# Kernel tuning notes

Hardware: AMD Instinct MI355X
Metric: run time of the kernel (lower is better)

Reference implementation:

```python
import jax, jax.numpy as jnp
import numpy as np

# ---- static config (mirrors init_kwargs) ----
B, T, H, W = 1, 3, 64, 64
NHEADS, CH = 4, 64
DIM = NHEADS * CH            # 256 = embed_dim*nheads*dim_mult
PS, WS = 7, 9                # patch size, search window
WSH = WS // 2
K_S, K_A = 16, 8             # search top-k, aggregation top-k
S0 = 2                       # stride0: query grid stride
SCALE = CH ** -0.5
NH, NW = (H - 1) // S0 + 1, (W - 1) // S0 + 1
Q = T * NH * NW              # ntotal queries


def reflect_idx(i, n):
    # dnls reflect_bounds: i<0 -> -i, i>=n -> 2(n-1)-i
    i = jnp.where(i < 0, -i, i)
    return jnp.where(i >= n, 2 * (n - 1) - i, i)


def sepconv(x, dw, pw, b):
    # ConvQKV branch: depthwise 3x3 + pointwise 1x1 (+bias). x: [N,C,H,W]
    y = jax.lax.conv_general_dilated(x, dw, (1, 1), 'SAME',
            dimension_numbers=('NCHW', 'OIHW', 'NCHW'),
            feature_group_count=x.shape[1])
    y = jax.lax.conv_general_dilated(y, pw, (1, 1), 'SAME',
            dimension_numbers=('NCHW', 'OIHW', 'NCHW'))
    return y + b[None, :, None, None]


def setup_inputs() -> dict:
    key = jax.random.key(0)
    ks = jax.random.split(key, 12)
    p = lambda k, s, sc=0.02: jax.random.normal(k, s, jnp.float32) * sc
    z = lambda s: jnp.zeros(s, jnp.float32)
    return {
        'vid':  jax.random.normal(ks[0], (B, T, DIM, H, W), jnp.float32),
        'q_dw': p(ks[1], (DIM, 1, 3, 3), 0.1), 'q_pw': p(ks[2], (DIM, DIM, 1, 1)), 'q_b': z((DIM,)),
        'k_dw': p(ks[3], (DIM, 1, 3, 3), 0.1), 'k_pw': p(ks[4], (DIM, DIM, 1, 1)), 'k_b': z((DIM,)),
        'v_dw': p(ks[5], (DIM, 1, 3, 3), 0.1), 'v_pw': p(ks[6], (DIM, DIM, 1, 1)), 'v_b': z((DIM,)),
        'proj_w': p(ks[7], (DIM, DIM)), 'proj_b': z((DIM,)),
    }


def reference(vid, q_dw, q_pw, q_b, k_dw, k_pw, k_b, v_dw, v_pw, v_b, proj_w, proj_b):
    x = vid.reshape(B * T, DIM, H, W)
    q = (sepconv(x, q_dw, q_pw, q_b) * SCALE).reshape(B, T, NHEADS, CH, H, W)
    k = sepconv(x, k_dw, k_pw, k_b).reshape(B, T, NHEADS, CH, H, W)
    v = sepconv(x, v_dw, v_pw, v_b).reshape(B, T, NHEADS, CH, H, W)

    # ---- non-local patch search (prod_with_heads), spatial window ws x ws, wt=0 ----
    yi, xi = jnp.arange(H), jnp.arange(W)
    ye = reflect_idx(jnp.arange(H + PS - 1), H)   # reflect-extended patch footprint
    xe = reflect_idx(jnp.arange(W + PS - 1), W)

    def offset_dists(dyo, dxo):
        # pixelwise q.k for k shifted by (dyo,dxo) with reflect bounds
        ks_ = k[..., reflect_idx(yi + dyo, H), :][..., reflect_idx(xi + dxo, W)]
        d = jnp.sum(q * ks_, axis=3)              # [B,T,HD,H,W]
        # separable ps x ps patch box-sum (patch anchored top-left)
        de = d[..., ye, :][..., xe]               # [B,T,HD,H+PS-1,W+PS-1]
        dsy = sum(de[..., p:p + H, :] for p in range(PS))
        return sum(dsy[..., p:p + W] for p in range(PS))   # [B,T,HD,H,W]

    offs = jnp.arange(WS) - WSH
    dyg, dxg = jnp.meshgrid(offs, offs, indexing='ij')
    dists_all = jax.vmap(offset_dists)(dyg.ravel(), dxg.ravel())  # [L,B,T,HD,H,W]

    gy, gx = jnp.arange(0, H, S0), jnp.arange(0, W, S0)
    dg = dists_all[..., gy, :][..., gx]           # [L,B,T,HD,NH,NW]
    dists = dg.transpose(1, 3, 2, 4, 5, 0).reshape(B, NHEADS, Q, WS * WS)
    vals, inds = jax.lax.top_k(dists, K_S)        # descending
    attn = jax.nn.softmax(vals, axis=-1)[..., :K_A]  # softmax over k_s, keep top k_a
    inds = inds[..., :K_A]

    # ---- weighted patch sum (wpsum) ----
    tq = jnp.repeat(jnp.arange(T), NH * NW)       # query coords [Q]
    yq = jnp.tile(jnp.repeat(gy, NW), T)
    xq = jnp.tile(jnp.tile(gx, NH), T)
    py = jnp.arange(PS)

    vflat = v.transpose(0, 2, 3, 1, 4, 5).reshape(B, NHEADS, CH, T * H * W)
    dy_k = inds // WS - WSH
    dx_k = inds % WS - WSH

    def gather_bh(vf, li):
        # vf: [CH, T*H*W], li: [Q,PS,PS] -> [CH,Q,PS,PS]
        return vf[:, li]

    acc = jnp.zeros((B, NHEADS, CH, Q, PS, PS), vid.dtype)
    for n in range(K_A):  # small fixed loop over neighbors
        yy = reflect_idx((yq[None, None, :] + dy_k[..., n])[..., None] + py, H)  # [B,HD,Q,PS]
        xx = reflect_idx((xq[None, None, :] + dx_k[..., n])[..., None] + py, W)
        lin = tq[None, None, :, None, None] * (H * W) + yy[..., :, None] * W + xx[..., None, :]
        vp = jax.vmap(jax.vmap(gather_bh))(vflat, lin)        # [B,HD,CH,Q,PS,PS]
        acc = acc + attn[..., n][:, :, None, :, None, None] * vp

    # ---- proj over concatenated heads per (query, patch pixel) ----
    pf = acc.transpose(0, 3, 4, 5, 1, 2).reshape(-1, DIM)     # [(B Q PS PS), DIM]
    pf = pf @ proj_w.T + proj_b

    # ---- iFoldz: overlap-add + per-pixel normalization ----
    patches = pf.reshape(B, Q, PS, PS, DIM).transpose(0, 4, 1, 2, 3)  # [B,DIM,Q,PS,PS]
    yyf = reflect_idx(yq[:, None] + py, H)
    xxf = reflect_idx(xq[:, None] + py, W)
    linf = (tq[:, None, None] * (H * W) + yyf[:, :, None] * W + xxf[:, None, :]).ravel()
    vacc = jnp.zeros((B, DIM, T * H * W), vid.dtype).at[:, :, linf].add(patches.reshape(B, DIM, -1))
    zv = jnp.zeros((T * H * W,), vid.dtype).at[linf].add(1.0)
    out = (vacc / zv).reshape(B, DIM, T, H, W).transpose(0, 2, 1, 3, 4)  # [B,T,DIM,H,W]
    return out
```

## Files before the change

kernel.cpp:

```cpp
#include <hip/hip_runtime.h>
#include <hip/hip_bf16.h>
#include <cmath>

#define TT 3
#define HH 64
#define WW 64
#define NPIX 4096
#define NHEADS 4
#define CHD 64
#define DIMD 256
#define PS 7
#define WS 9
#define WSH 4
#define KS 16
#define KA 8
#define NG 32
#define QTOT 3072
#define NOFF 81
#define SCALE 0.125f

#define OFF_DW   ((size_t)0)
#define OFF_Q    ((size_t)9437184)
#define OFF_K    ((size_t)12582912)
#define OFF_V    ((size_t)15728640)
#define OFF_D    ((size_t)18874368)
#define OFF_DG   ((size_t)22855680)
#define OFF_ATTN ((size_t)23851008)
#define OFF_INDS ((size_t)23949312)
#define OFF_VACC ((size_t)24047616)

__device__ __forceinline__ int reflect_i(int i, int n) {
  i = i < 0 ? -i : i;
  return i >= n ? 2 * (n - 1) - i : i;
}

__global__ void k_dw(const float* __restrict__ vid,
                     const float* __restrict__ qdw, const float* __restrict__ kdw,
                     const float* __restrict__ vdw, float* __restrict__ dw) {
  int plane = blockIdx.x;
  int ch = plane & 255;
  const float* src = vid + (size_t)plane * NPIX;
  float wq[9], wk[9], wv[9];
#pragma unroll
  for (int i = 0; i < 9; i++) { wq[i] = qdw[ch*9+i]; wk[i] = kdw[ch*9+i]; wv[i] = vdw[ch*9+i]; }
  int x = threadIdx.x, ty = threadIdx.y;
  for (int yb = 0; yb < 16; ++yb) {
    int y = yb * 4 + ty;
    float aq = 0, ak = 0, av = 0;
#pragma unroll
    for (int a = 0; a < 3; a++) {
      int yy = y + a - 1;
      if (yy < 0 || yy >= HH) continue;
#pragma unroll
      for (int b = 0; b < 3; b++) {
        int xx = x + b - 1;
        if (xx < 0 || xx >= WW) continue;
        float xv = src[yy * WW + xx];
        aq += xv * wq[a*3+b]; ak += xv * wk[a*3+b]; av += xv * wv[a*3+b];
      }
    }
    size_t o = (size_t)plane * NPIX + y * WW + x;
    dw[o] = aq;
    dw[(size_t)3145728 + o] = ak;
    dw[(size_t)6291456 + o] = av;
  }
}

__global__ void k_pw(const float* __restrict__ dw,
                     const float* __restrict__ qpw, const float* __restrict__ qb,
                     const float* __restrict__ kpw, const float* __restrict__ kb,
                     const float* __restrict__ vpw, const float* __restrict__ vb,
                     float* __restrict__ qo, float* __restrict__ ko, float* __restrict__ vo) {
  int type = blockIdx.z / 3, t = blockIdx.z % 3;
  const float* W   = type == 0 ? qpw : (type == 1 ? kpw : vpw);
  const float* bia = type == 0 ? qb  : (type == 1 ? kb  : vb);
  const float* A = dw + (size_t)type * 3145728 + (size_t)t * 1048576;
  int p0 = blockIdx.x * 64, o0 = blockIdx.y * 64;

  __shared__ float sW[16][68];
  __shared__ float sA[16][68];

  int tid = threadIdx.x;
  int ty = tid >> 4, tx = tid & 15;
  int wrow = tid >> 2, wcol = tid & 3;
  int arow = tid >> 4, acol = tid & 15;

  float acc[4][4] = {};

  for (int k0 = 0; k0 < 256; k0 += 16) {
    float4 w4 = *(const float4*)&W[(size_t)(o0 + wrow) * 256 + k0 + wcol * 4];
    float4 a4 = *(const float4*)&A[(size_t)(k0 + arow) * NPIX + p0 + acol * 4];
    __syncthreads();
    sW[wcol * 4 + 0][wrow] = w4.x;
    sW[wcol * 4 + 1][wrow] = w4.y;
    sW[wcol * 4 + 2][wrow] = w4.z;
    sW[wcol * 4 + 3][wrow] = w4.w;
    *(float4*)&sA[arow][acol * 4] = a4;
    __syncthreads();
#pragma unroll
    for (int kk = 0; kk < 16; kk++) {
      float4 av = *(const float4*)&sW[kk][ty * 4];
      float4 bv = *(const float4*)&sA[kk][tx * 4];
      acc[0][0] += av.x * bv.x; acc[0][1] += av.x * bv.y; acc[0][2] += av.x * bv.z; acc[0][3] += av.x * bv.w;
      acc[1][0] += av.y * bv.x; acc[1][1] += av.y * bv.y; acc[1][2] += av.y * bv.z; acc[1][3] += av.y * bv.w;
      acc[2][0] += av.z * bv.x; acc[2][1] += av.z * bv.y; acc[2][2] += av.z * bv.z; acc[2][3] += av.z * bv.w;
      acc[3][0] += av.w * bv.x; acc[3][1] += av.w * bv.y; acc[3][2] += av.w * bv.z; acc[3][3] += av.w * bv.w;
    }
  }

  int obase = o0 + ty * 4, pbase = p0 + tx * 4;
  if (type == 2) {
#pragma unroll
    for (int j = 0; j < 4; j++) {
      float4 ov = make_float4(acc[0][j] + bia[obase + 0],
                              acc[1][j] + bia[obase + 1],
                              acc[2][j] + bia[obase + 2],
                              acc[3][j] + bia[obase + 3]);
      *(float4*)&vo[((size_t)t * NPIX + pbase + j) * 256 + obase] = ov;
    }
  } else {
    float* dst = (type == 0) ? qo : ko;
    float sc = (type == 0) ? SCALE : 1.0f;
#pragma unroll
    for (int i = 0; i < 4; i++) {
      float bb = bia[obase + i];
      float4 ov = make_float4((acc[i][0] + bb) * sc, (acc[i][1] + bb) * sc,
                              (acc[i][2] + bb) * sc, (acc[i][3] + bb) * sc);
      *(float4*)&dst[((size_t)t * 256 + obase + i) * NPIX + pbase] = ov;
    }
  }
}

__global__ void k_dist(const float* __restrict__ q, const float* __restrict__ k,
                       float* __restrict__ D) {
  int b = blockIdx.x;
  int y = b & 63, th = b >> 6;
  int t = th >> 2, h = th & 3;
  __shared__ float sQ[64][64];
  __shared__ float sK[64][64];
  int tid = threadIdx.x;
  int x = tid & 63, w = tid >> 6;
  const float* qp = q + ((size_t)t * 256 + h * 64) * NPIX;
  const float* kp = k + ((size_t)t * 256 + h * 64) * NPIX;
  for (int i = tid; i < 4096; i += 256)
    sQ[i >> 6][i & 63] = qp[(size_t)(i >> 6) * NPIX + y * WW + (i & 63)];
  for (int dyi = 0; dyi < 9; ++dyi) {
    int yk = reflect_i(y + dyi - 4, HH);
    __syncthreads();
    for (int i = tid; i < 4096; i += 256)
      sK[i >> 6][i & 63] = kp[(size_t)(i >> 6) * NPIX + yk * WW + (i & 63)];
    __syncthreads();
    for (int dxi = w; dxi < 9; dxi += 4) {
      int xk = reflect_i(x + dxi - 4, WW);
      float s = 0.f;
#pragma unroll 16
      for (int c = 0; c < 64; c++) s += sQ[c][x] * sK[c][xk];
      D[((size_t)(dyi * 9 + dxi) * 12 + th) * NPIX + y * WW + x] = s;
    }
  }
}

__global__ void k_box(const float* __restrict__ D, float* __restrict__ DG) {
  int th = blockIdx.x, n = blockIdx.y;
  int t = th >> 2, h = th & 3;
  __shared__ float sD[4096];
  int tid = threadIdx.x;
  const float* Dp = D + ((size_t)n * 12 + th) * NPIX;
  for (int i = tid; i < 4096; i += 256) sD[i] = Dp[i];
  __syncthreads();
  for (int qi = tid; qi < 1024; qi += 256) {
    int gy = qi >> 5, gx = qi & 31;
    int yq = gy * 2, xq = gx * 2;
    float s = 0.f;
#pragma unroll
    for (int py = 0; py < 7; py++) {
      int ry = yq + py; ry = ry >= HH ? 126 - ry : ry;
      const float* row = sD + ry * WW;
#pragma unroll
      for (int px = 0; px < 7; px++) {
        int rx = xq + px; rx = rx >= WW ? 126 - rx : rx;
        s += row[rx];
      }
    }
    DG[((size_t)h * QTOT + t * 1024 + qi) * NOFF + n] = s;
  }
}

__global__ void k_topk(const float* __restrict__ DG, float* __restrict__ attn,
                       int* __restrict__ inds) {
  int r = blockIdx.x * 256 + threadIdx.x;
  if (r >= NHEADS * QTOT) return;
  const float* row = DG + (size_t)r * NOFF;
  float dv[NOFF];
#pragma unroll
  for (int i = 0; i < NOFF; i++) dv[i] = row[i];
  float vals[KS]; int idx[KS];
#pragma unroll
  for (int s = 0; s < KS; s++) {
    float best = -1e30f; int bi = 0;
#pragma unroll
    for (int i = 0; i < NOFF; i++) {
      if (dv[i] > best) { best = dv[i]; bi = i; }
    }
    vals[s] = best; idx[s] = bi;
#pragma unroll
    for (int i = 0; i < NOFF; i++) dv[i] = (i == bi) ? -1e30f : dv[i];
  }
  float m = vals[0], den = 0.f, e[KS];
#pragma unroll
  for (int s = 0; s < KS; s++) { e[s] = expf(vals[s] - m); den += e[s]; }
  float inv = 1.f / den;
#pragma unroll
  for (int s = 0; s < KA; s++) {
    attn[(size_t)r * KA + s] = e[s] * inv;
    inds[(size_t)r * KA + s] = idx[s];
  }
}

#define NW 7
__global__ void k_agg(const float* __restrict__ v, const float* __restrict__ attn,
                      const int* __restrict__ inds, float* __restrict__ vacc) {
  int xg = blockIdx.x, y = blockIdx.y, t = blockIdx.z;
  int x0 = xg * 4;

  int g0 = max(0, (y - 5) >> 1), g1 = y >> 1;
  int ndir = g1 - g0 + 1;
  int yr = 126 - y;
  int r0 = (yr - 5) >> 1;
  int ny = ndir + (y >= 58 ? (min(31, yr >> 1) - r0 + 1) : 0);

  int gxw0 = max(0, (x0 - 5) >> 1);
  int gxw1 = (x0 + 3) >= 58 ? 31 : ((x0 + 3) >> 1);
  int nw = gxw1 - gxw0 + 1;

  __shared__ float wt[7][NW][4][8];
  __shared__ int2  rc[7][NW][4][8];

  int tid = threadIdx.x;
  {
    int iy = tid / (NW * 4);
    int rem = tid - iy * (NW * 4);
    int gxi = rem >> 2, h = rem & 3;
    if (iy < ny && gxi < nw) {
      int gy, py;
      if (iy < ndir) { gy = g0 + iy; py = y - 2 * gy; }
      else           { gy = r0 + (iy - ndir); py = yr - 2 * gy; }
      int gx = gxw0 + gxi;
      size_t r = (size_t)(h * QTOT + t * 1024 + gy * 32 + gx);
      float4 w0 = *(const float4*)(attn + r * KA);
      float4 w1 = *(const float4*)(attn + r * KA + 4);
      int4 i0 = *(const int4*)(inds + r * KA);
      int4 i1 = *(const int4*)(inds + r * KA + 4);
      int ids[8] = {i0.x, i0.y, i0.z, i0.w, i1.x, i1.y, i1.z, i1.w};
      float ww[8] = {w0.x, w0.y, w0.z, w0.w, w1.x, w1.y, w1.z, w1.w};
#pragma unroll
      for (int n = 0; n < 8; n++) {
        int dy = ids[n] / 9 - 4, dx = ids[n] % 9 - 4;
        int row = 2 * gy + dy + py;
        row = row < 0 ? -row : row;
        row = min(row, 126 - row);
        wt[iy][gxi][h][n] = ww[n];
        rc[iy][gxi][h][n] = make_int2(row << 16, 2 * gx + dx);
      }
    }
  }
  __syncthreads();

  int wv = tid >> 6, lane = tid & 63;
  int x = x0 + wv;
  int h = lane >> 4;
  const char* vB = (const char*)v + (size_t)t * ((size_t)NPIX * DIMD * 4)
                   + (unsigned)(lane * 16);

  int a0 = max(0, (x - 5) >> 1), a1 = x >> 1;
  int xr = 126 - x;
  int b0 = (xr - 5) >> 1, b1 = min(31, xr >> 1);
  bool has_refl = (x >= 58);

  float4 acc = make_float4(0.f, 0.f, 0.f, 0.f);
  for (int iy = 0; iy < ny; ++iy) {
    for (int g = a0; g <= a1; ++g) {
      int gxi = g - gxw0, px = x - 2 * g;
      const float* w8 = wt[iy][gxi][h];
      const int2* r8 = rc[iy][gxi][h];
#pragma unroll
      for (int n = 0; n < 8; n++) {
        float w = w8[n]; int2 e = r8[n];
        int col = e.y + px;
        col = col < 0 ? -col : col;
        col = min(col, 126 - col);
        float4 vv = *(const float4*)(vB + (unsigned)(e.x + (col << 10)));
        acc.x += w * vv.x; acc.y += w * vv.y; acc.z += w * vv.z; acc.w += w * vv.w;
      }
    }
    if (has_refl) {
      for (int g = b0; g <= b1; ++g) {
        int gxi = g - gxw0, px = xr - 2 * g;
        const float* w8 = wt[iy][gxi][h];
        const int2* r8 = rc[iy][gxi][h];
#pragma unroll
        for (int n = 0; n < 8; n++) {
          float w = w8[n]; int2 e = r8[n];
          int col = e.y + px;
          col = col < 0 ? -col : col;
          col = min(col, 126 - col);
          float4 vv = *(const float4*)(vB + (unsigned)(e.x + (col << 10)));
          acc.x += w * vv.x; acc.y += w * vv.y; acc.z += w * vv.z; acc.w += w * vv.w;
        }
      }
    }
  }
  float* oP = vacc + ((size_t)t * NPIX + (size_t)y * WW + x) * DIMD + lane * 4;
  *(float4*)oP = acc;
}

__device__ __forceinline__ int cov_count(int i) {
  int d = (i >> 1) - max(0, (i - 5) >> 1) + 1;
  if (i >= 58) { int r = 126 - i; d += min(31, r >> 1) - ((r - 5) >> 1) + 1; }
  return d;
}

__global__ void k_proj(const float* __restrict__ vacc,
                       const float* __restrict__ pw, const float* __restrict__ pb,
                       float* __restrict__ out) {
  int p0 = blockIdx.x * 64;
  int d0 = blockIdx.y * 64;

  __shared__ float sW[16][68];
  __shared__ float sV[16][68];

  int tid = threadIdx.x;
  int ty = tid >> 4, tx = tid & 15;
  int row = tid >> 2, col = tid & 3;

  float acc[4][4] = {};

  for (int k0 = 0; k0 < 256; k0 += 16) {
    float4 w4 = *(const float4*)&pw[(size_t)(d0 + row) * 256 + k0 + col * 4];
    float4 v4 = *(const float4*)&vacc[(size_t)(p0 + row) * 256 + k0 + col * 4];
    __syncthreads();
    sW[col * 4 + 0][row] = w4.x;
    sW[col * 4 + 1][row] = w4.y;
    sW[col * 4 + 2][row] = w4.z;
    sW[col * 4 + 3][row] = w4.w;
    sV[col * 4 + 0][row] = v4.x;
    sV[col * 4 + 1][row] = v4.y;
    sV[col * 4 + 2][row] = v4.z;
    sV[col * 4 + 3][row] = v4.w;
    __syncthreads();
#pragma unroll
    for (int kk = 0; kk < 16; kk++) {
      float4 av = *(const float4*)&sW[kk][ty * 4];
      float4 bv = *(const float4*)&sV[kk][tx * 4];
      acc[0][0] += av.x * bv.x; acc[0][1] += av.x * bv.y; acc[0][2] += av.x * bv.z; acc[0][3] += av.x * bv.w;
      acc[1][0] += av.y * bv.x; acc[1][1] += av.y * bv.y; acc[1][2] += av.y * bv.z; acc[1][3] += av.y * bv.w;
      acc[2][0] += av.z * bv.x; acc[2][1] += av.z * bv.y; acc[2][2] += av.z * bv.z; acc[2][3] += av.z * bv.w;
      acc[3][0] += av.w * bv.x; acc[3][1] += av.w * bv.y; acc[3][2] += av.w * bv.z; acc[3][3] += av.w * bv.w;
    }
  }

  int dbase = d0 + ty * 4, pbase = p0 + tx * 4;
  float izv[4];
#pragma unroll
  for (int j = 0; j < 4; j++) {
    int pl = (pbase + j) & 4095;
    int yy = pl >> 6, xx = pl & 63;
    izv[j] = 1.0f / (float)(cov_count(yy) * cov_count(xx));
  }
  int t = pbase >> 12, pl0 = pbase & 4095;
#pragma unroll
  for (int i = 0; i < 4; i++) {
    int d = dbase + i;
    float bb = pb[d];
    float4 ov = make_float4(acc[i][0] * izv[0] + bb, acc[i][1] * izv[1] + bb,
                            acc[i][2] * izv[2] + bb, acc[i][3] * izv[3] + bb);
    *(float4*)&out[((size_t)t * 256 + d) * NPIX + pl0] = ov;
  }
}

extern "C" void kernel_launch(void* const* d_in, const int* in_sizes, int n_in,
                              void* d_out, int out_size, void* d_ws, size_t ws_size,
                              hipStream_t stream) {
  const float* vid = (const float*)d_in[0];
  const float* qdw = (const float*)d_in[1];
  const float* qpw = (const float*)d_in[2];
  const float* qb  = (const float*)d_in[3];
  const float* kdw = (const float*)d_in[4];
  const float* kpw = (const float*)d_in[5];
  const float* kb  = (const float*)d_in[6];
  const float* vdw = (const float*)d_in[7];
  const float* vpw = (const float*)d_in[8];
  const float* vb  = (const float*)d_in[9];
  const float* pw  = (const float*)d_in[10];
  const float* pb  = (const float*)d_in[11];
  float* out = (float*)d_out;
  float* ws = (float*)d_ws;

  float* dwb  = ws + OFF_DW;
  float* qbuf = ws + OFF_Q;
  float* kbuf = ws + OFF_K;
  float* vbuf = ws + OFF_V;
  float* Dbuf = ws + OFF_D;
  float* DG   = ws + OFF_DG;
  float* attn = ws + OFF_ATTN;
  int*   inds = (int*)(ws + OFF_INDS);
  float* vacc = ws + OFF_VACC;

  k_dw<<<dim3(768), dim3(64, 4), 0, stream>>>(vid, qdw, kdw, vdw, dwb);
  k_pw<<<dim3(64, 4, 9), 256, 0, stream>>>(dwb, qpw, qb, kpw, kb, vpw, vb,
                                           qbuf, kbuf, vbuf);
  k_dist<<<dim3(768), 256, 0, stream>>>(qbuf, kbuf, Dbuf);
  k_box<<<dim3(12, 81), 256, 0, stream>>>(Dbuf, DG);
  k_topk<<<dim3(48), 256, 0, stream>>>(DG, attn, inds);
  k_agg<<<dim3(16, 64, 3), 256, 0, stream>>>(vbuf, attn, inds, vacc);
  k_proj<<<dim3(192, 4), 256, 0, stream>>>(vacc, pw, pb, out);
}
```

Measured before the change: 299.1 us.

## Parallelize top-k selection with one wavefront per row using shuffle argmax

The top-k kernel used one thread per query row, doing 16 sequential passes over 81 register-held distances. It now assigns a 64-lane wavefront per row: each lane holds up to two packed keys (order-preserving float bits plus index), and a butterfly shuffle reduction finds the max for each of the 16 selections. The grid grows from 48 to 3072 blocks to raise parallelism and remove the serial, register-heavy scan. Ties resolve to the lower index, as before, and only lane 0 computes the softmax and writes results.

```diff
diff --git a/kernel.cpp b/kernel.cpp
--- a/kernel.cpp
+++ b/kernel.cpp
@@ -188,32 +188,50 @@
 
 __global__ void k_topk(const float* __restrict__ DG, float* __restrict__ attn,
                        int* __restrict__ inds) {
-  int r = blockIdx.x * 256 + threadIdx.x;
-  if (r >= NHEADS * QTOT) return;
+  int lane = threadIdx.x & 63;
+  int r = blockIdx.x * 4 + (threadIdx.x >> 6);
   const float* row = DG + (size_t)r * NOFF;
-  float dv[NOFF];
-#pragma unroll
-  for (int i = 0; i < NOFF; i++) dv[i] = row[i];
+
+  float v0 = row[lane];
+  float v1 = (lane < NOFF - 64) ? row[64 + lane] : 0.f;
+
+  auto mono = [](float f) -> unsigned {
+    unsigned b = __float_as_uint(f);
+    return (b & 0x80000000u) ? ~b : (b | 0x80000000u);
+  };
+  unsigned long long k0 = ((unsigned long long)mono(v0) << 7) | (unsigned)(127 - lane);
+  unsigned long long k1 = (lane < NOFF - 64)
+      ? (((unsigned long long)mono(v1) << 7) | (unsigned)(127 - 64 - lane))
+      : 0ull;
+
   float vals[KS]; int idx[KS];
 #pragma unroll
   for (int s = 0; s < KS; s++) {
-    float best = -1e30f; int bi = 0;
-#pragma unroll
-    for (int i = 0; i < NOFF; i++) {
-      if (dv[i] > best) { best = dv[i]; bi = i; }
-    }
-    vals[s] = best; idx[s] = bi;
-#pragma unroll
-    for (int i = 0; i < NOFF; i++) dv[i] = (i == bi) ? -1e30f : dv[i];
-  }
-  float m = vals[0], den = 0.f, e[KS];
-#pragma unroll
-  for (int s = 0; s < KS; s++) { e[s] = expf(vals[s] - m); den += e[s]; }
-  float inv = 1.f / den;
-#pragma unroll
-  for (int s = 0; s < KA; s++) {
-    attn[(size_t)r * KA + s] = e[s] * inv;
-    inds[(size_t)r * KA + s] = idx[s];
+    unsigned long long k = k0 > k1 ? k0 : k1;
+#pragma unroll
+    for (int m = 32; m >= 1; m >>= 1) {
+      unsigned long long o = __shfl_xor(k, m, 64);
+      if (o > k) k = o;
+    }
+    int wi = 127 - (int)(k & 127);
+    unsigned mb = (unsigned)(k >> 7);
+    unsigned vb = (mb & 0x80000000u) ? (mb ^ 0x80000000u) : ~mb;
+    vals[s] = __uint_as_float(vb);
+    idx[s] = wi;
+    if (wi == lane) k0 = 0ull;
+    else if (wi == 64 + lane) k1 = 0ull;
+  }
+
+  if (lane == 0) {
+    float m = vals[0], den = 0.f, e[KS];
+#pragma unroll
+    for (int s = 0; s < KS; s++) { e[s] = expf(vals[s] - m); den += e[s]; }
+    float inv = 1.f / den;
+#pragma unroll
+    for (int s = 0; s < KA; s++) {
+      attn[(size_t)r * KA + s] = e[s] * inv;
+      inds[(size_t)r * KA + s] = idx[s];
+    }
   }
 }
 
@@ -411,7 +429,7 @@
                                            qbuf, kbuf, vbuf);
   k_dist<<<dim3(768), 256, 0, stream>>>(qbuf, kbuf, Dbuf);
   k_box<<<dim3(12, 81), 256, 0, stream>>>(Dbuf, DG);
-  k_topk<<<dim3(48), 256, 0, stream>>>(DG, attn, inds);
+  k_topk<<<dim3(3072), 256, 0, stream>>>(DG, attn, inds);
   k_agg<<<dim3(16, 64, 3), 256, 0, stream>>>(vbuf, attn, inds, vacc);
   k_proj<<<dim3(192, 4), 256, 0, stream>>>(vacc, pw, pb, out);
 }
```

Result: no change. 303.0 us (+1.3%).
